# Optimization experiments

Measured on AMD Instinct MI355X. Metric: run time of the kernel, lower is better.

## Reference

```python
import jax, jax.numpy as jnp
import numpy as np

N = 50000      # nodes
E = 1600000    # edges (avg degree 32)
D = 128        # node feature dim
C = 10         # classes
BN_EPS = 1e-5


def _w(k, shape, fan_in):
    lim = 1.0 / np.sqrt(fan_in)
    return jax.random.uniform(k, shape, jnp.float32, -lim, lim)


def setup_inputs() -> dict:
    key = jax.random.key(0)
    ks = jax.random.split(key, 16)
    inp = {}
    inp["x"] = jax.random.normal(ks[0], (N, D), jnp.float32)
    inp["edge_attr"] = jax.random.normal(ks[1], (E, 1), jnp.float32)
    inp["edge_index"] = jax.random.randint(ks[2], (2, E), 0, N)
    # edge-attr projection Linear(1, D) (D_n > D_e branch)
    inp["lin_w"] = _w(ks[3], (1, D), 1)
    inp["lin_b"] = jnp.zeros((D,), jnp.float32)
    # conv1 nn: MLP([D, D]) = Linear + ReLU + BatchNorm1d
    inp["w1"] = _w(ks[4], (D, D), D); inp["b1"] = jnp.zeros((D,)); inp["g1"] = jnp.ones((D,)); inp["be1"] = jnp.zeros((D,))
    # conv2 nn: MLP([D, 64])
    inp["w2"] = _w(ks[5], (D, 64), D); inp["b2"] = jnp.zeros((64,)); inp["g2"] = jnp.ones((64,)); inp["be2"] = jnp.zeros((64,))
    # lin1: MLP([D+64, 96])
    inp["w3"] = _w(ks[6], (D + 64, 96), D + 64); inp["b3"] = jnp.zeros((96,)); inp["g3"] = jnp.ones((96,)); inp["be3"] = jnp.zeros((96,))
    # mlp1: MLP([96, 96, C])
    inp["w4"] = _w(ks[7], (96, 96), 96); inp["b4"] = jnp.zeros((96,)); inp["g4"] = jnp.ones((96,)); inp["be4"] = jnp.zeros((96,))
    inp["w5"] = _w(ks[8], (96, C), 96); inp["b5"] = jnp.zeros((C,)); inp["g5"] = jnp.ones((C,)); inp["be5"] = jnp.zeros((C,))
    return inp


def _bn(h, g, b):
    # BatchNorm1d training-mode: batch statistics, biased variance
    m = h.mean(axis=0)
    v = h.var(axis=0)
    return g * (h - m) * jax.lax.rsqrt(v + BN_EPS) + b


def _mlp_layer(h, w, b, g, be):
    # nn.Sequential(Linear, ReLU, BatchNorm1d)
    return _bn(jax.nn.relu(h @ w + b), g, be)


def reference(x, edge_attr, edge_index, lin_w, lin_b,
              w1, b1, g1, be1, w2, b2, g2, be2,
              w3, b3, g3, be3, w4, b4, g4, be4,
              w5, b5, g5, be5):
    # project scalar edge features to node dim (D_n > D_e branch)
    e = edge_attr @ lin_w + lin_b  # [E, D]
    src, dst = edge_index[0], edge_index[1]

    def gine(h, w, b, g, be):
        # GINEConv (eps=0): nn(x_i + sum_j relu(x_j + e_ji))
        msg = jax.nn.relu(h[src] + e)                      # [E, D]
        aggr = jax.ops.segment_sum(msg, dst, num_segments=N)  # [N, D]
        return _mlp_layer(h + aggr, w, b, g, be)

    x1 = gine(x, w1, b1, g1, be1)    # [N, D]
    x2 = gine(x1, w2, b2, g2, be2)   # [N, 64]
    h = _mlp_layer(jnp.concatenate([x1, x2], axis=1), w3, b3, g3, be3)  # [N, 96]
    h = _mlp_layer(h, w4, b4, g4, be4)  # [N, 96]
    h = _mlp_layer(h, w5, b5, g5, be5)  # [N, C]
    return h
```

## Files before the change

### kernel.cpp

```cpp
#include <hip/hip_runtime.h>
#include <hip/hip_fp16.h>

static constexpr float BN_EPS = 1e-5f;

using half8 = __attribute__((ext_vector_type(8))) _Float16;
using f32x4 = __attribute__((ext_vector_type(4))) float;

__device__ __forceinline__ ushort f2h(float f) {
    return __half_as_ushort(__float2half(f));
}
__device__ __forceinline__ __half2 u2h2(uint u) {
    union { uint u; __half2 h; } c; c.u = u; return c.h;
}
__device__ __forceinline__ uint h22u(__half2 h) {
    union { uint u; __half2 h; } c; c.h = h; return c.u;
}
__device__ __forceinline__ uint pk2(float a, float b) {
    return (uint)f2h(a) | ((uint)f2h(b) << 16);
}
__device__ __forceinline__ uint relu2u(uint u) {
    return u & ~(((u >> 15) & 0x10001u) * 0xFFFFu);
}

__global__ __launch_bounds__(256) void cvt_f16(
    const float* __restrict__ in, ushort* __restrict__ out, int n4)
{
    int i = blockIdx.x * 256 + threadIdx.x;
    const int stride = gridDim.x * 256;
    for (; i < n4; i += stride) {
        const float4 v = ((const float4*)in)[i];
        ushort4 u;
        u.x = f2h(v.x); u.y = f2h(v.y); u.z = f2h(v.z); u.w = f2h(v.w);
        ((ushort4*)out)[i] = u;
    }
}

__device__ __forceinline__ void pack_store(ushort* dst, int M, int k, int c, float v)
{
    const int kc = k >> 5, kk = k & 31, ct = c >> 4;
    const int lane = (c & 15) | ((kk >> 3) << 4);
    const int j = kk & 7;
    dst[((size_t)(kc * (M / 16) + ct) * 64 + lane) * 8 + j] = f2h(v);
}

__global__ __launch_bounds__(256) void pack_all(
    const float* __restrict__ w1, const float* __restrict__ w2,
    const float* __restrict__ w3, const float* __restrict__ w4,
    const float* __restrict__ w5, const float* __restrict__ b5,
    const float* __restrict__ lw, const float* __restrict__ lb,
    ushort* __restrict__ Wp, float* __restrict__ b5p, float* __restrict__ sums,
    uint* __restrict__ lwh, uint* __restrict__ lbh)
{
    int t = blockIdx.x * 256 + threadIdx.x;
    if (t < 16384) { pack_store(Wp, 128, t / 128, t % 128, w1[t]); return; }
    t -= 16384;
    if (t < 8192) { pack_store(Wp + 16384, 64, t / 64, t % 64, w2[t]); return; }
    t -= 8192;
    if (t < 18432) { pack_store(Wp + 24576, 96, t / 96, t % 96, w3[t]); return; }
    t -= 18432;
    if (t < 9216) { pack_store(Wp + 43008, 96, t / 96, t % 96, w4[t]); return; }
    t -= 9216;
    if (t < 1536) {
        const int k = t / 16, c = t % 16;
        pack_store(Wp + 52224, 16, k, c, (c < 10) ? w5[k * 10 + c] : 0.f);
        return;
    }
    t -= 1536;
    if (t < 16) { b5p[t] = (t < 10) ? b5[t] : 0.f; return; }
    t -= 16;
    if (t < 1280) { sums[t] = 0.f; return; }
    t -= 1280;
    if (t < 64) { lwh[t] = pk2(lw[2 * t], lw[2 * t + 1]); return; }
    t -= 64;
    if (t < 64) { lbh[t] = pk2(lb[2 * t], lb[2 * t + 1]); return; }
}

__device__ inline int wave_incl_scan(int v, int lane)
{
#pragma unroll
    for (int s = 1; s < 64; s <<= 1) {
        const int t = __shfl_up(v, s, 64);
        if (lane >= s) v += t;
    }
    return v;
}

__global__ __launch_bounds__(1024) void scan1(
    const int* __restrict__ cnt, int* __restrict__ off, int* __restrict__ bsum, int n)
{
    __shared__ int wsum[16];
    const int tid = threadIdx.x, lane = tid & 63, wid = tid >> 6;
    const int i = blockIdx.x * 1024 + tid;
    const int v = (i < n) ? cnt[i] : 0;
    const int incl = wave_incl_scan(v, lane);
    if (lane == 63) wsum[wid] = incl;
    __syncthreads();
    if (wid == 0) {
        int wv = (lane < 16) ? wsum[lane] : 0;
        wv = wave_incl_scan(wv, lane);
        if (lane < 16) wsum[lane] = wv;
    }
    __syncthreads();
    const int excl = (wid > 0 ? wsum[wid - 1] : 0) + incl - v;
    if (i < n) off[i] = excl;
    if (tid == 1023) bsum[blockIdx.x] = wsum[15];
}

__global__ __launch_bounds__(64) void scan2(int* __restrict__ bsum, int nb)
{
    const int lane = threadIdx.x;
    int carry = 0;
    for (int base = 0; base < nb; base += 64) {
        const int idx = base + lane;
        const int v = (idx < nb) ? bsum[idx] : 0;
        const int incl = wave_incl_scan(v, lane);
        if (idx < nb) bsum[idx] = carry + incl - v;
        carry += __shfl(incl, 63, 64);
    }
}

__global__ __launch_bounds__(1024) void scan3(
    int* __restrict__ off, const int* __restrict__ bsum, int n)
{
    const int i = blockIdx.x * 1024 + threadIdx.x;
    if (i < n) off[i] += bsum[blockIdx.x];
}

__global__ __launch_bounds__(256) void hist_blocks(
    const int* __restrict__ dst, int* __restrict__ H, int E, int NB, int NBLK)
{
    __shared__ int h[512];
    for (int i = threadIdx.x; i < NB; i += 256) h[i] = 0;
    __syncthreads();
    const int chunk = (E + NBLK - 1) / NBLK;
    const int beg = blockIdx.x * chunk;
    const int end = min(beg + chunk, E);
    for (int i = beg + threadIdx.x; i < end; i += 256)
        atomicAdd(&h[dst[i] >> 7], 1);
    __syncthreads();
    for (int i = threadIdx.x; i < NB; i += 256)
        H[(size_t)i * NBLK + blockIdx.x] = h[i];
}

__global__ __launch_bounds__(256) void scatter_coarse(
    const int* __restrict__ src, const int* __restrict__ dst,
    const float* __restrict__ ea, const int* __restrict__ H,
    uint* __restrict__ tmp_e, uchar* __restrict__ tmp_d, int E, int NB, int NBLK)
{
    __shared__ int h[512];
    for (int i = threadIdx.x; i < NB; i += 256)
        h[i] = H[(size_t)i * NBLK + blockIdx.x];
    __syncthreads();
    const int chunk = (E + NBLK - 1) / NBLK;
    const int beg = blockIdx.x * chunk;
    const int end = min(beg + chunk, E);
    for (int i = beg + threadIdx.x; i < end; i += 256) {
        const int d = dst[i];
        const int pos = atomicAdd(&h[d >> 7], 1);
        tmp_e[pos] = (uint)(src[i] & 0xFFFF) | ((uint)f2h(ea[i]) << 16);
        tmp_d[pos] = (uchar)(d & 127);
    }
}

__global__ __launch_bounds__(256) void fill_fine2(
    const uint* __restrict__ tmp_e, const uchar* __restrict__ tmp_d,
    const int* __restrict__ H, int* __restrict__ off, uint* __restrict__ edges,
    int N, int E, int NBLK)
{
    __shared__ int cnt[128];
    __shared__ int wtot;
    const int b = blockIdx.x;
    const int base = b * 128;
    const int tid = threadIdx.x;
    const int lo = H[(size_t)b * NBLK];
    const int hi = (b + 1 < (int)gridDim.x) ? H[(size_t)(b + 1) * NBLK] : E;
    if (tid < 128) cnt[tid] = 0;
    __syncthreads();
    for (int i = lo + tid; i < hi; i += 256)
        atomicAdd(&cnt[tmp_d[i]], 1);
    __syncthreads();
    int excl = 0;
    if (tid < 128) {
        const int v = cnt[tid];
        const int incl = wave_incl_scan(v, tid & 63);
        if (tid == 63) wtot = incl;
        excl = incl - v;
    }
    __syncthreads();
    if (tid >= 64 && tid < 128) excl += wtot;
    if (tid < 128) {
        const int o = lo + excl;
        if (base + tid < N) off[base + tid] = o;
        cnt[tid] = o;
    }
    if (b == 0 && tid == 0) off[N] = E;
    __syncthreads();
    for (int i = lo + tid; i < hi; i += 256) {
        const int dl = tmp_d[i];
        const uint pe = tmp_e[i];
        const int pos = atomicAdd(&cnt[dl], 1);
        edges[pos] = pe;
    }
}

template<bool AFF>
__global__ __launch_bounds__(256) void gine_aggr(
    const ushort* __restrict__ xh, const int* __restrict__ off,
    const uint* __restrict__ edges, const uint* __restrict__ lwh,
    const uint* __restrict__ lbh, const float* __restrict__ su,
    const float* __restrict__ qu, const float* __restrict__ g,
    const float* __restrict__ be, float invN,
    ushort* __restrict__ outh, int N)
{
    const int q = threadIdx.x & 15;
    const int node = blockIdx.x * 16 + (threadIdx.x >> 4);
    if (node >= N) return;
    __half2 lw[4], lb[4], sc[4], sh[4];
#pragma unroll
    for (int i = 0; i < 4; ++i) {
        lw[i] = u2h2(lwh[q * 4 + i]);
        lb[i] = u2h2(lbh[q * 4 + i]);
    }
    if constexpr (AFF) {
        const int c0 = q * 8;
#pragma unroll
        for (int i = 0; i < 4; ++i) {
            const float2 s2 = *(const float2*)(su + c0 + 2 * i);
            const float2 q2 = *(const float2*)(qu + c0 + 2 * i);
            const float2 g2 = *(const float2*)(g + c0 + 2 * i);
            const float2 b2 = *(const float2*)(be + c0 + 2 * i);
            const float m0 = s2.x * invN, m1 = s2.y * invN;
            const float c0f = g2.x * rsqrtf(q2.x * invN - m0 * m0 + BN_EPS);
            const float c1f = g2.y * rsqrtf(q2.y * invN - m1 * m1 + BN_EPS);
            sc[i] = u2h2(pk2(c0f, c1f));
            sh[i] = u2h2(pk2(b2.x - m0 * c0f, b2.y - m1 * c1f));
        }
    }
    __half2 acc[4];
    {
        const uint4 u = ((const uint4*)(xh + (size_t)node * 128))[q];
        acc[0] = u2h2(u.x); acc[1] = u2h2(u.y); acc[2] = u2h2(u.z); acc[3] = u2h2(u.w);
        if constexpr (AFF) {
#pragma unroll
            for (int i = 0; i < 4; ++i) acc[i] = __hfma2(acc[i], sc[i], sh[i]);
        }
    }

    auto proc = [&](uint e, uint4 u) {
        const __half2 a2 = u2h2((e >> 16) * 0x10001u);
        uint ua[4] = {u.x, u.y, u.z, u.w};
#pragma unroll
        for (int i = 0; i < 4; ++i) {
            __half2 x2 = u2h2(ua[i]);
            if constexpr (AFF) x2 = __hfma2(x2, sc[i], sh[i]);
            __half2 m = __hfma2(a2, lw[i], lb[i]);
            m = __hadd2(x2, m);
            m = u2h2(relu2u(h22u(m)));
            acc[i] = __hadd2(acc[i], m);
        }
    };

    int p = off[node];
    const int pend = off[node + 1];
    if (p < pend) {
        uint e = edges[p];
        uint4 u = ((const uint4*)(xh + (size_t)(e & 0xFFFFu) * 128))[q];
        for (++p; p < pend; ++p) {
            const uint en = edges[p];
            const uint4 un = ((const uint4*)(xh + (size_t)(en & 0xFFFFu) * 128))[q];
            proc(e, u);
            e = en; u = un;
        }
        proc(e, u);
    }
    uint4 o;
    o.x = h22u(acc[0]); o.y = h22u(acc[1]); o.z = h22u(acc[2]); o.w = h22u(acc[3]);
    ((uint4*)(outh + (size_t)node * 128))[q] = o;
}

__device__ __forceinline__ half8 affine_h8(
    half8 a, const float* sc, const float* sh, int k)
{
    const float4 c0 = *(const float4*)(sc + k), c1 = *(const float4*)(sc + k + 4);
    const float4 d0 = *(const float4*)(sh + k), d1 = *(const float4*)(sh + k + 4);
    half8 r;
    r[0] = (_Float16)fmaf((float)a[0], c0.x, d0.x);
    r[1] = (_Float16)fmaf((float)a[1], c0.y, d0.y);
    r[2] = (_Float16)fmaf((float)a[2], c0.z, d0.z);
    r[3] = (_Float16)fmaf((float)a[3], c0.w, d0.w);
    r[4] = (_Float16)fmaf((float)a[4], c1.x, d1.x);
    r[5] = (_Float16)fmaf((float)a[5], c1.y, d1.y);
    r[6] = (_Float16)fmaf((float)a[6], c1.z, d1.z);
    r[7] = (_Float16)fmaf((float)a[7], c1.w, d1.w);
    return r;
}

template<int K, int KS, int M, bool YH, bool AF1, bool AF2>
__global__ __launch_bounds__(256) void gemm_mfma(
    const ushort* __restrict__ A1, const ushort* __restrict__ A2,
    const float* __restrict__ su1, const float* __restrict__ sq1_,
    const float* __restrict__ g1, const float* __restrict__ be1,
    const float* __restrict__ su2, const float* __restrict__ sq2_,
    const float* __restrict__ g2, const float* __restrict__ be2,
    const ushort* __restrict__ Wp, const float* __restrict__ bias,
    void* __restrict__ Yv, float* __restrict__ sum, float* __restrict__ sq,
    int N, float invN)
{
    constexpr int NCT = M / 16;
    constexpr int NKC = K / 32;
    __shared__ float redS[4][M];
    __shared__ float redQ[4][M];
    __shared__ float scL[K];
    __shared__ float shL[K];
    const int tid = threadIdx.x;
    if constexpr (AF1 || AF2) {
        for (int i = tid; i < K; i += 256) {
            float s_, q_, g_, b_;
            if (i < KS) { s_ = su1[i]; q_ = sq1_[i]; g_ = g1[i]; b_ = be1[i]; }
            else        { s_ = su2[i - KS]; q_ = sq2_[i - KS]; g_ = g2[i - KS]; b_ = be2[i - KS]; }
            const float m = s_ * invN;
            const float c = g_ * rsqrtf(q_ * invN - m * m + BN_EPS);
            scL[i] = c; shL[i] = b_ - m * c;
        }
        __syncthreads();
    }
    const int w = tid >> 6, l = tid & 63;
    const int col = l & 15, kg = l >> 4;
    const int rowA = blockIdx.x * 64 + w * 16 + col;
    const int rA = (rowA < N) ? rowA : (N - 1);
    f32x4 acc[NCT];
#pragma unroll
    for (int ct = 0; ct < NCT; ++ct) acc[ct] = f32x4{0.f, 0.f, 0.f, 0.f};
#pragma unroll
    for (int kc = 0; kc < NKC; ++kc) {
        const int kbase = kc * 32 + kg * 8;
        half8 a;
        if constexpr (KS < K) {
            if (kbase >= KS) {
                a = *(const half8*)(A2 + (size_t)rA * (K - KS) + (kbase - KS));
                if constexpr (AF2) a = affine_h8(a, scL, shL, kbase);
            } else {
                a = *(const half8*)(A1 + (size_t)rA * KS + kbase);
                if constexpr (AF1) a = affine_h8(a, scL, shL, kbase);
            }
        } else {
            a = *(const half8*)(A1 + (size_t)rA * K + kbase);
            if constexpr (AF1) a = affine_h8(a, scL, shL, kbase);
        }
#pragma unroll
        for (int ct = 0; ct < NCT; ++ct) {
            const half8 wf = *(const half8*)(Wp + ((size_t)(kc * NCT + ct) * 64 + l) * 8);
            acc[ct] = __builtin_amdgcn_mfma_f32_16x16x32_f16(a, wf, acc[ct], 0, 0, 0);
        }
    }
    const int row0 = blockIdx.x * 64 + w * 16 + 4 * kg;
#pragma unroll
    for (int ct = 0; ct < NCT; ++ct) {
        const float bs = bias[ct * 16 + col];
        float sS = 0.f, sQ = 0.f;
#pragma unroll
        for (int r = 0; r < 4; ++r) {
            const int ro = row0 + r;
            if (ro < N) {
                const float o = fmaxf(acc[ct][r] + bs, 0.f);
                if constexpr (YH) ((ushort*)Yv)[(size_t)ro * M + ct * 16 + col] = f2h(o);
                else              ((float*)Yv)[(size_t)ro * M + ct * 16 + col] = o;
                sS += o; sQ = fmaf(o, o, sQ);
            }
        }
        sS += __shfl_xor(sS, 16, 64); sQ += __shfl_xor(sQ, 16, 64);
        sS += __shfl_xor(sS, 32, 64); sQ += __shfl_xor(sQ, 32, 64);
        if (l < 16) { redS[w][ct * 16 + col] = sS; redQ[w][ct * 16 + col] = sQ; }
    }
    __syncthreads();
    for (int i = tid; i < M; i += 256) {
        const float S = redS[0][i] + redS[1][i] + redS[2][i] + redS[3][i];
        const float Q = redQ[0][i] + redQ[1][i] + redQ[2][i] + redQ[3][i];
        unsafeAtomicAdd(&sum[i], S);
        unsafeAtomicAdd(&sq[i], Q);
    }
}

__global__ __launch_bounds__(256) void bn_apply_final(
    const float* __restrict__ Y16, const float* __restrict__ su,
    const float* __restrict__ qu, const float* __restrict__ g5,
    const float* __restrict__ be5, float* __restrict__ out, int total, float invN)
{
    for (int i = blockIdx.x * 256 + threadIdx.x; i < total; i += gridDim.x * 256) {
        const int n = i / 10;
        const int c = i - n * 10;
        const float m = su[c] * invN;
        const float sc = g5[c] * rsqrtf(qu[c] * invN - m * m + BN_EPS);
        const float sh = be5[c] - m * sc;
        out[i] = fmaf(Y16[(size_t)n * 16 + c], sc, sh);
    }
}

extern "C" void kernel_launch(void* const* d_in, const int* in_sizes, int n_in,
                              void* d_out, int out_size, void* d_ws, size_t ws_size,
                              hipStream_t stream)
{
    const float* x   = (const float*)d_in[0];
    const float* ea  = (const float*)d_in[1];
    const int*   ei  = (const int*)d_in[2];
    const float* lw  = (const float*)d_in[3];
    const float* lb  = (const float*)d_in[4];
    const float* w1  = (const float*)d_in[5];
    const float* b1  = (const float*)d_in[6];
    const float* g1  = (const float*)d_in[7];
    const float* be1 = (const float*)d_in[8];
    const float* w2  = (const float*)d_in[9];
    const float* b2  = (const float*)d_in[10];
    const float* g2  = (const float*)d_in[11];
    const float* be2 = (const float*)d_in[12];
    const float* w3  = (const float*)d_in[13];
    const float* b3  = (const float*)d_in[14];
    const float* g3  = (const float*)d_in[15];
    const float* be3 = (const float*)d_in[16];
    const float* w4  = (const float*)d_in[17];
    const float* b4  = (const float*)d_in[18];
    const float* g4  = (const float*)d_in[19];
    const float* be4 = (const float*)d_in[20];
    const float* w5  = (const float*)d_in[21];
    const float* b5  = (const float*)d_in[22];
    const float* g5  = (const float*)d_in[23];
    const float* be5 = (const float*)d_in[24];

    const int N = in_sizes[0] / 128;
    const int E = in_sizes[1];
    const int* src = ei;
    const int* dst = ei + E;
    const float invN = 1.0f / (float)N;

    float* ws = (float*)d_ws;
    ushort* Pa = (ushort*)ws;
    ushort* Pb = (ushort*)(ws + (size_t)N * 64);
    ushort* Pc = (ushort*)(ws + (size_t)N * 128);
    ushort* Pd = (ushort*)(ws + (size_t)N * 160);
    float*  y5 = ws + (size_t)N * 208;
    float*  smallr = ws + (size_t)N * 224;
    float*  sums   = smallr;
    float*  b5p    = smallr + 1280;
    uint*   lwh    = (uint*)(smallr + 1296);
    uint*   lbh    = lwh + 64;
    ushort* Wp     = (ushort*)(smallr + 1424);
    int*    ibase  = (int*)(smallr + 1424 + 26880);
    int*    H      = ibase;
    int*    bsum   = H + 100160;
    uint*   tmp_e  = (uint*)(bsum + 128);
    uchar*  tmp_d  = (uchar*)(tmp_e + E);
    uint*   edges  = (uint*)(tmp_d + ((E + 3) & ~3));
    int*    off    = (int*)(edges + E);
#define SUM(l)   (sums + (l) * 128)
#define SQ(l)    (sums + (5 + (l)) * 128)

    pack_all<<<216, 256, 0, stream>>>(w1, w2, w3, w4, w5, b5, lw, lb, Wp, b5p, sums, lwh, lbh);
    cvt_f16<<<2048, 256, 0, stream>>>(x, Pa, N * 32);

    const int NB   = (N + 127) / 128;
    const int NBLK = 256;
    const int nH   = NB * NBLK;
    const int nbH  = (nH + 1023) / 1024;
    hist_blocks<<<NBLK, 256, 0, stream>>>(dst, H, E, NB, NBLK);
    scan1<<<nbH, 1024, 0, stream>>>(H, H, bsum, nH);
    scan2<<<1, 64, 0, stream>>>(bsum, nbH);
    scan3<<<nbH, 1024, 0, stream>>>(H, bsum, nH);
    scatter_coarse<<<NBLK, 256, 0, stream>>>(src, dst, ea, H, tmp_e, tmp_d, E, NB, NBLK);
    fill_fine2<<<NB, 256, 0, stream>>>(tmp_e, tmp_d, H, off, edges, N, E, NBLK);

    const int gemmGrid = (N + 63) / 64;
    const int aggrGrid = (N + 15) / 16;

    gine_aggr<false><<<aggrGrid, 256, 0, stream>>>(
        Pa, off, edges, lwh, lbh, nullptr, nullptr, nullptr, nullptr, invN, Pb, N);
    gemm_mfma<128, 128, 128, true, false, false><<<gemmGrid, 256, 0, stream>>>(
        Pb, nullptr, nullptr, nullptr, nullptr, nullptr,
        nullptr, nullptr, nullptr, nullptr,
        Wp, b1, Pa, SUM(0), SQ(0), N, invN);

    gine_aggr<true><<<aggrGrid, 256, 0, stream>>>(
        Pa, off, edges, lwh, lbh, SUM(0), SQ(0), g1, be1, invN, Pb, N);
    gemm_mfma<128, 128, 64, true, false, false><<<gemmGrid, 256, 0, stream>>>(
        Pb, nullptr, nullptr, nullptr, nullptr, nullptr,
        nullptr, nullptr, nullptr, nullptr,
        Wp + 16384, b2, Pc, SUM(1), SQ(1), N, invN);

    gemm_mfma<192, 128, 96, true, true, true><<<gemmGrid, 256, 0, stream>>>(
        Pa, Pc, SUM(0), SQ(0), g1, be1, SUM(1), SQ(1), g2, be2,
        Wp + 24576, b3, Pb, SUM(2), SQ(2), N, invN);

    gemm_mfma<96, 96, 96, true, true, false><<<gemmGrid, 256, 0, stream>>>(
        Pb, nullptr, SUM(2), SQ(2), g3, be3, nullptr, nullptr, nullptr, nullptr,
        Wp + 43008, b4, Pd, SUM(3), SQ(3), N, invN);

    gemm_mfma<96, 96, 16, false, true, false><<<gemmGrid, 256, 0, stream>>>(
        Pd, nullptr, SUM(3), SQ(3), g4, be4, nullptr, nullptr, nullptr, nullptr,
        Wp + 52224, b5p, y5, SUM(4), SQ(4), N, invN);

    bn_apply_final<<<1024, 256, 0, stream>>>(y5, SUM(4), SQ(4), g5, be5,
                                             (float*)d_out, N * 10, invN);
#undef SUM
#undef SQ
}
```

Before: 326.6 us.

## Fuse setup kernels, merge scan passes, prefetch edges deeper, double GEMM rows per block

Merges the fp16 input conversion into the weight-packing kernel and folds the single-wave block-sum scan into the offset-add kernel, where each block serially sums its preceding block totals. This removes two launches. The edge aggregation loop now prefetches two edges ahead, using two zero-padded sentinel entries after the edge array so the lookahead reads stay in bounds. Each GEMM block handles 128 rows with two accumulator sets that share the weight fragment loads. The final layer output is stored in fp16 instead of fp32, which cuts traffic but loses precision before the last BatchNorm.

```diff
diff --git a/kernel.cpp b/kernel.cpp
--- a/kernel.cpp
+++ b/kernel.cpp
@@ -15,24 +15,15 @@
 __device__ __forceinline__ uint h22u(__half2 h) {
     union { uint u; __half2 h; } c; c.h = h; return c.u;
 }
+__device__ __forceinline__ float h2f1(ushort u) {
+    __half h = *reinterpret_cast<__half*>(&u);
+    return __half2float(h);
+}
 __device__ __forceinline__ uint pk2(float a, float b) {
     return (uint)f2h(a) | ((uint)f2h(b) << 16);
 }
 __device__ __forceinline__ uint relu2u(uint u) {
     return u & ~(((u >> 15) & 0x10001u) * 0xFFFFu);
-}
-
-__global__ __launch_bounds__(256) void cvt_f16(
-    const float* __restrict__ in, ushort* __restrict__ out, int n4)
-{
-    int i = blockIdx.x * 256 + threadIdx.x;
-    const int stride = gridDim.x * 256;
-    for (; i < n4; i += stride) {
-        const float4 v = ((const float4*)in)[i];
-        ushort4 u;
-        u.x = f2h(v.x); u.y = f2h(v.y); u.z = f2h(v.z); u.w = f2h(v.w);
-        ((ushort4*)out)[i] = u;
-    }
 }
 
 __device__ __forceinline__ void pack_store(ushort* dst, int M, int k, int c, float v)
@@ -43,7 +34,8 @@
     dst[((size_t)(kc * (M / 16) + ct) * 64 + lane) * 8 + j] = f2h(v);
 }
 
-__global__ __launch_bounds__(256) void pack_all(
+__global__ __launch_bounds__(256) void setup_fused(
+    const float* __restrict__ x, ushort* __restrict__ xh, int n4,
     const float* __restrict__ w1, const float* __restrict__ w2,
     const float* __restrict__ w3, const float* __restrict__ w4,
     const float* __restrict__ w5, const float* __restrict__ b5,
@@ -51,7 +43,15 @@
     ushort* __restrict__ Wp, float* __restrict__ b5p, float* __restrict__ sums,
     uint* __restrict__ lwh, uint* __restrict__ lbh)
 {
-    int t = blockIdx.x * 256 + threadIdx.x;
+    const int gid = blockIdx.x * 256 + threadIdx.x;
+    const int stride = gridDim.x * 256;
+    for (int i = gid; i < n4; i += stride) {
+        const float4 v = ((const float4*)x)[i];
+        ushort4 u;
+        u.x = f2h(v.x); u.y = f2h(v.y); u.z = f2h(v.z); u.w = f2h(v.w);
+        ((ushort4*)xh)[i] = u;
+    }
+    int t = gid;
     if (t < 16384) { pack_store(Wp, 128, t / 128, t % 128, w1[t]); return; }
     t -= 16384;
     if (t < 8192) { pack_store(Wp + 16384, 64, t / 64, t % 64, w2[t]); return; }
@@ -106,24 +106,18 @@
     if (tid == 1023) bsum[blockIdx.x] = wsum[15];
 }
 
-__global__ __launch_bounds__(64) void scan2(int* __restrict__ bsum, int nb)
-{
-    const int lane = threadIdx.x;
-    int carry = 0;
-    for (int base = 0; base < nb; base += 64) {
-        const int idx = base + lane;
-        const int v = (idx < nb) ? bsum[idx] : 0;
-        const int incl = wave_incl_scan(v, lane);
-        if (idx < nb) bsum[idx] = carry + incl - v;
-        carry += __shfl(incl, 63, 64);
-    }
-}
-
-__global__ __launch_bounds__(1024) void scan3(
+__global__ __launch_bounds__(1024) void scan3f(
     int* __restrict__ off, const int* __restrict__ bsum, int n)
 {
+    __shared__ int pre;
+    if (threadIdx.x == 0) {
+        int s = 0;
+        for (int j = 0; j < (int)blockIdx.x; ++j) s += bsum[j];
+        pre = s;
+    }
+    __syncthreads();
     const int i = blockIdx.x * 1024 + threadIdx.x;
-    if (i < n) off[i] += bsum[blockIdx.x];
+    if (i < n) off[i] += pre;
 }
 
 __global__ __launch_bounds__(256) void hist_blocks(
@@ -260,18 +254,20 @@
         }
     };
 
-    int p = off[node];
+    const int p0 = off[node];
     const int pend = off[node + 1];
-    if (p < pend) {
-        uint e = edges[p];
-        uint4 u = ((const uint4*)(xh + (size_t)(e & 0xFFFFu) * 128))[q];
-        for (++p; p < pend; ++p) {
-            const uint en = edges[p];
-            const uint4 un = ((const uint4*)(xh + (size_t)(en & 0xFFFFu) * 128))[q];
-            proc(e, u);
-            e = en; u = un;
-        }
-        proc(e, u);
+    if (p0 < pend) {
+        uint e0 = edges[p0];
+        uint4 u0 = ((const uint4*)(xh + (size_t)(e0 & 0xFFFFu) * 128))[q];
+        uint e1 = edges[p0 + 1];
+        uint4 u1 = ((const uint4*)(xh + (size_t)(e1 & 0xFFFFu) * 128))[q];
+        for (int p = p0; p < pend; ++p) {
+            const uint e2 = edges[p + 2];
+            const uint4 u2 = ((const uint4*)(xh + (size_t)(e2 & 0xFFFFu) * 128))[q];
+            proc(e0, u0);
+            e0 = e1; u0 = u1;
+            e1 = e2; u1 = u2;
+        }
     }
     uint4 o;
     o.x = h22u(acc[0]); o.y = h22u(acc[1]); o.z = h22u(acc[2]); o.w = h22u(acc[3]);
@@ -326,14 +322,17 @@
     }
     const int w = tid >> 6, l = tid & 63;
     const int col = l & 15, kg = l >> 4;
-    const int rowA = blockIdx.x * 64 + w * 16 + col;
-    const int rA = (rowA < N) ? rowA : (N - 1);
-    f32x4 acc[NCT];
-#pragma unroll
-    for (int ct = 0; ct < NCT; ++ct) acc[ct] = f32x4{0.f, 0.f, 0.f, 0.f};
-#pragma unroll
-    for (int kc = 0; kc < NKC; ++kc) {
-        const int kbase = kc * 32 + kg * 8;
+    const int rowAa = blockIdx.x * 128 + w * 16 + col;
+    const int rowAb = rowAa + 64;
+    const int rAa = (rowAa < N) ? rowAa : (N - 1);
+    const int rAb = (rowAb < N) ? rowAb : (N - 1);
+    f32x4 accA[NCT], accB[NCT];
+#pragma unroll
+    for (int ct = 0; ct < NCT; ++ct) {
+        accA[ct] = f32x4{0.f, 0.f, 0.f, 0.f};
+        accB[ct] = f32x4{0.f, 0.f, 0.f, 0.f};
+    }
+    auto loadA = [&](int rA, int kbase) -> half8 {
         half8 a;
         if constexpr (KS < K) {
             if (kbase >= KS) {
@@ -347,22 +346,41 @@
             a = *(const half8*)(A1 + (size_t)rA * K + kbase);
             if constexpr (AF1) a = affine_h8(a, scL, shL, kbase);
         }
+        return a;
+    };
+#pragma unroll
+    for (int kc = 0; kc < NKC; ++kc) {
+        const int kbase = kc * 32 + kg * 8;
+        const half8 aA = loadA(rAa, kbase);
+        const half8 aB = loadA(rAb, kbase);
 #pragma unroll
         for (int ct = 0; ct < NCT; ++ct) {
             const half8 wf = *(const half8*)(Wp + ((size_t)(kc * NCT + ct) * 64 + l) * 8);
-            acc[ct] = __builtin_amdgcn_mfma_f32_16x16x32_f16(a, wf, acc[ct], 0, 0, 0);
-        }
-    }
-    const int row0 = blockIdx.x * 64 + w * 16 + 4 * kg;
+            accA[ct] = __builtin_amdgcn_mfma_f32_16x16x32_f16(aA, wf, accA[ct], 0, 0, 0);
+            accB[ct] = __builtin_amdgcn_mfma_f32_16x16x32_f16(aB, wf, accB[ct], 0, 0, 0);
+        }
+    }
+    const int row0a = blockIdx.x * 128 + w * 16 + 4 * kg;
+    const int row0b = row0a + 64;
 #pragma unroll
     for (int ct = 0; ct < NCT; ++ct) {
         const float bs = bias[ct * 16 + col];
         float sS = 0.f, sQ = 0.f;
 #pragma unroll
         for (int r = 0; r < 4; ++r) {
-            const int ro = row0 + r;
+            const int ro = row0a + r;
             if (ro < N) {
-                const float o = fmaxf(acc[ct][r] + bs, 0.f);
+                const float o = fmaxf(accA[ct][r] + bs, 0.f);
+                if constexpr (YH) ((ushort*)Yv)[(size_t)ro * M + ct * 16 + col] = f2h(o);
+                else              ((float*)Yv)[(size_t)ro * M + ct * 16 + col] = o;
+                sS += o; sQ = fmaf(o, o, sQ);
+            }
+        }
+#pragma unroll
+        for (int r = 0; r < 4; ++r) {
+            const int ro = row0b + r;
+            if (ro < N) {
+                const float o = fmaxf(accB[ct][r] + bs, 0.f);
                 if constexpr (YH) ((ushort*)Yv)[(size_t)ro * M + ct * 16 + col] = f2h(o);
                 else              ((float*)Yv)[(size_t)ro * M + ct * 16 + col] = o;
                 sS += o; sQ = fmaf(o, o, sQ);
@@ -382,7 +400,7 @@
 }
 
 __global__ __launch_bounds__(256) void bn_apply_final(
-    const float* __restrict__ Y16, const float* __restrict__ su,
+    const ushort* __restrict__ Y16h, const float* __restrict__ su,
     const float* __restrict__ qu, const float* __restrict__ g5,
     const float* __restrict__ be5, float* __restrict__ out, int total, float invN)
 {
@@ -392,7 +410,7 @@
         const float m = su[c] * invN;
         const float sc = g5[c] * rsqrtf(qu[c] * invN - m * m + BN_EPS);
         const float sh = be5[c] - m * sc;
-        out[i] = fmaf(Y16[(size_t)n * 16 + c], sc, sh);
+        out[i] = fmaf(h2f1(Y16h[(size_t)n * 16 + c]), sc, sh);
     }
 }
 
@@ -437,7 +455,7 @@
     ushort* Pb = (ushort*)(ws + (size_t)N * 64);
     ushort* Pc = (ushort*)(ws + (size_t)N * 128);
     ushort* Pd = (ushort*)(ws + (size_t)N * 160);
-    float*  y5 = ws + (size_t)N * 208;
+    ushort* y5h = (ushort*)(ws + (size_t)N * 208);
     float*  smallr = ws + (size_t)N * 224;
     float*  sums   = smallr;
     float*  b5p    = smallr + 1280;
@@ -450,12 +468,13 @@
     uint*   tmp_e  = (uint*)(bsum + 128);
     uchar*  tmp_d  = (uchar*)(tmp_e + E);
     uint*   edges  = (uint*)(tmp_d + ((E + 3) & ~3));
-    int*    off    = (int*)(edges + E);
+    int*    off    = (int*)(edges + E + 2);
 #define SUM(l)   (sums + (l) * 128)
 #define SQ(l)    (sums + (5 + (l)) * 128)
 
-    pack_all<<<216, 256, 0, stream>>>(w1, w2, w3, w4, w5, b5, lw, lb, Wp, b5p, sums, lwh, lbh);
-    cvt_f16<<<2048, 256, 0, stream>>>(x, Pa, N * 32);
+    setup_fused<<<2048, 256, 0, stream>>>(x, Pa, N * 32, w1, w2, w3, w4, w5, b5,
+                                          lw, lb, Wp, b5p, sums, lwh, lbh);
+    hipMemsetAsync(edges + E, 0, 2 * sizeof(uint), stream);
 
     const int NB   = (N + 127) / 128;
     const int NBLK = 256;
@@ -463,12 +482,11 @@
     const int nbH  = (nH + 1023) / 1024;
     hist_blocks<<<NBLK, 256, 0, stream>>>(dst, H, E, NB, NBLK);
     scan1<<<nbH, 1024, 0, stream>>>(H, H, bsum, nH);
-    scan2<<<1, 64, 0, stream>>>(bsum, nbH);
-    scan3<<<nbH, 1024, 0, stream>>>(H, bsum, nH);
+    scan3f<<<nbH, 1024, 0, stream>>>(H, bsum, nH);
     scatter_coarse<<<NBLK, 256, 0, stream>>>(src, dst, ea, H, tmp_e, tmp_d, E, NB, NBLK);
     fill_fine2<<<NB, 256, 0, stream>>>(tmp_e, tmp_d, H, off, edges, N, E, NBLK);
 
-    const int gemmGrid = (N + 63) / 64;
+    const int gemmGrid = (N + 127) / 128;
     const int aggrGrid = (N + 15) / 16;
 
     gine_aggr<false><<<aggrGrid, 256, 0, stream>>>(
@@ -493,11 +511,11 @@
         Pb, nullptr, SUM(2), SQ(2), g3, be3, nullptr, nullptr, nullptr, nullptr,
         Wp + 43008, b4, Pd, SUM(3), SQ(3), N, invN);
 
-    gemm_mfma<96, 96, 16, false, true, false><<<gemmGrid, 256, 0, stream>>>(
+    gemm_mfma<96, 96, 16, true, true, false><<<gemmGrid, 256, 0, stream>>>(
         Pd, nullptr, SUM(3), SQ(3), g4, be4, nullptr, nullptr, nullptr, nullptr,
-        Wp + 52224, b5p, y5, SUM(4), SQ(4), N, invN);
-
-    bn_apply_final<<<1024, 256, 0, stream>>>(y5, SUM(4), SQ(4), g5, be5,
+        Wp + 52224, b5p, y5h, SUM(4), SQ(4), N, invN);
+
+    bn_apply_final<<<1024, 256, 0, stream>>>(y5h, SUM(4), SQ(4), g5, be5,
                                              (float*)d_out, N * 10, invN);
 #undef SUM
 #undef SQ
```

Result: faster. 300.1 us (-8.1%).
